# Performance work log

Hardware: AMD Instinct MI355X
Metric: run time of the kernel (lower is better)

Reference implementation:

```python
import jax, jax.numpy as jnp
import numpy as np

B, C_IN, T = 32, 192, 8192
H, N_PH, OUT = 192, 1024, 4
EPS = 1e-5


def setup_inputs() -> dict:
    key = jax.random.key(0)
    ks = jax.random.split(key, 12)
    s = 0.02
    return {
        "x": jax.random.normal(ks[0], (B, C_IN, T), jnp.float32),
        "x_mask": jnp.ones((B, 1, N_PH), jnp.float32),
        "w": jax.random.randint(ks[1], (B, 1, N_PH), 0, 8, jnp.int32),
        "pre_w": jax.random.normal(ks[2], (H, C_IN), jnp.float32) * s,
        "pre_b": jnp.zeros((H,), jnp.float32),
        "conv0_w": jax.random.normal(ks[3], (H, H, 3), jnp.float32) * s,
        "conv0_b": jnp.zeros((H,), jnp.float32),
        "ln0_g": jnp.ones((H,), jnp.float32),
        "ln0_b": jnp.zeros((H,), jnp.float32),
        "conv1_w": jax.random.normal(ks[4], (H, H, 3), jnp.float32) * s,
        "conv1_b": jnp.zeros((H,), jnp.float32),
        "ln1_g": jnp.ones((H,), jnp.float32),
        "ln1_b": jnp.zeros((H,), jnp.float32),
        "lin_w": jax.random.normal(ks[5], (OUT, H), jnp.float32) * s,
        "lin_b": jnp.zeros((OUT,), jnp.float32),
    }


def _segment_mean(x, w2):
    # x: [B, C, T] frames; w2: [B, n_ph] int durations.
    # Faithful to the torch double loop: phoneme j pools frames
    # [cumsum(w)[j-1] : cumsum(w)[j]); w==0 -> zeros.
    ends = jnp.cumsum(w2, axis=1)                      # [B, n_ph]
    t = jnp.arange(x.shape[2], dtype=ends.dtype)       # [T]
    ph_id = jax.vmap(lambda e: jnp.searchsorted(e, t, side="right"))(ends)  # [B, T]
    # segment sums over frames; extra segment n_ph catches out-of-range frames
    sums = jax.vmap(lambda xt, ids: jax.ops.segment_sum(xt, ids, num_segments=N_PH + 1))(
        x.transpose(0, 2, 1), ph_id
    )                                                  # [B, n_ph+1, C]
    sums = sums[:, :N_PH].transpose(0, 2, 1)           # [B, C, n_ph]
    denom = jnp.maximum(w2, 1).astype(x.dtype)[:, None, :]
    return jnp.where(w2[:, None, :] > 0, sums / denom, 0.0)


def _conv3(x, k, b):
    y = jax.lax.conv_general_dilated(x, k, (1,), [(1, 1)],
                                     dimension_numbers=("NCH", "OIH", "NCH"))
    return y + b[None, :, None]


def _ln(x, g, b):
    # channel-dim LayerNorm for [B, C, T] (VITS modules.LayerNorm)
    m = jnp.mean(x, axis=1, keepdims=True)
    v = jnp.mean(jnp.square(x - m), axis=1, keepdims=True)
    return (x - m) * jax.lax.rsqrt(v + EPS) * g[None, :, None] + b[None, :, None]


def reference(x, x_mask, w, pre_w, pre_b, conv0_w, conv0_b, ln0_g, ln0_b,
              conv1_w, conv1_b, ln1_g, ln1_b, lin_w, lin_b):
    w2 = w.reshape(w.shape[0], -1).astype(jnp.int32)
    spec = _segment_mean(x, w2)                                 # [B, C_in, n_ph]
    h = jnp.einsum("bct,hc->bht", spec, pre_w) + pre_b[None, :, None]
    # block 0: conv -> relu -> LN (dropout is identity at eval), mask before each layer
    h = _conv3(h * x_mask, conv0_w, conv0_b)
    h = jax.nn.relu(h * x_mask)
    h = _ln(h * x_mask, ln0_g, ln0_b)
    h = h * x_mask  # dropout(p=0.1) at eval = identity; mask still applied
    # block 1
    h = _conv3(h * x_mask, conv1_w, conv1_b)
    h = jax.nn.relu(h * x_mask)
    h = _ln(h * x_mask, ln1_g, ln1_b)
    h = h * x_mask
    p = jnp.einsum("bht,oh->bot", h, lin_w) + lin_b[None, :, None]
    return p * x_mask
```

## Files before the change

kernel.cpp:

```cpp
#include <hip/hip_runtime.h>
#include <hip/hip_bf16.h>

#define B 32
#define C_IN 192
#define T 8192
#define H 192
#define N_PH 1024
#define OUT 4
#define ROW_MAX 7168
#define PROWS (N_PH + 2)
#define ROWP (2 * H)

typedef __attribute__((ext_vector_type(8))) short short8;
typedef __attribute__((ext_vector_type(4))) float f32x4;
typedef unsigned short ushort_t;

__device__ inline ushort_t f2bf(float f) {
    unsigned u = __builtin_bit_cast(unsigned, f);
    unsigned r = u + 0x7fffu + ((u >> 16) & 1u);
    return (ushort_t)(r >> 16);
}
__device__ inline float bf2f(ushort_t h) {
    unsigned u = ((unsigned)h) << 16;
    return __builtin_bit_cast(float, u);
}
__device__ inline void split_bf(float x, ushort_t& hi, ushort_t& lo) {
    hi = f2bf(x);
    lo = f2bf(x - bf2f(hi));
}

__global__ __launch_bounds__(256) void segmean_kernel(const float* __restrict__ x,
                                                      const int* __restrict__ wdur,
                                                      float* __restrict__ spec) {
    int bc = blockIdx.x;
    int b = bc / C_IN;
    int c = bc % C_IN;
    __shared__ int e_s[N_PH];
    __shared__ int part[256];
    __shared__ float row[ROW_MAX];
    int tid = threadIdx.x;
    int4 w4 = ((const int4*)(wdur + b * N_PH))[tid];
    int c0 = w4.x, c1 = c0 + w4.y, c2 = c1 + w4.z, c3 = c2 + w4.w;
    part[tid] = c3;
    __syncthreads();
    for (int off = 1; off < 256; off <<= 1) {
        int v = (tid >= off) ? part[tid - off] : 0;
        __syncthreads();
        part[tid] += v;
        __syncthreads();
    }
    int pre = tid ? part[tid - 1] : 0;
    e_s[4 * tid + 0] = pre + c0;
    e_s[4 * tid + 1] = pre + c1;
    e_s[4 * tid + 2] = pre + c2;
    e_s[4 * tid + 3] = pre + c3;
    __syncthreads();
    int emax = e_s[N_PH - 1];
    const float4* xr4 = (const float4*)(x + ((size_t)b * C_IN + c) * T);
    float4* row4 = (float4*)row;
    int nv = (emax + 3) >> 2;
    for (int t = tid; t < nv; t += 256) row4[t] = xr4[t];
    __syncthreads();
    float* sp = spec + ((size_t)b * C_IN + c) * N_PH;
    for (int j = tid; j < N_PH; j += 256) {
        int s0 = j ? e_s[j - 1] : 0;
        int e0 = e_s[j];
        float sum = 0.f;
        for (int t = s0; t < e0; ++t) sum += row[t];
        sp[j] = (e0 > s0) ? sum / (float)(e0 - s0) : 0.f;
    }
}

__global__ __launch_bounds__(256) void transpose_spec_kernel(const float* __restrict__ spec,
                                                             ushort_t* __restrict__ specT) {
    int jt = blockIdx.x * 32;
    int ct = (blockIdx.y % (C_IN / 32)) * 32;
    int b  = blockIdx.y / (C_IN / 32);
    __shared__ float tile[32][33];
    int tx = threadIdx.x & 31;
    int ty = threadIdx.x >> 5;
    const float* sb = spec + ((size_t)b * C_IN + ct) * N_PH + jt;
    for (int r = ty; r < 32; r += 8) tile[r][tx] = sb[(size_t)r * N_PH + tx];
    __syncthreads();
    ushort_t* ob = specT + ((size_t)b * N_PH + jt) * ROWP + ct;
    for (int r = ty; r < 32; r += 8) {
        ushort_t hi, lo;
        split_bf(tile[tx][r], hi, lo);
        ob[(size_t)r * ROWP + tx] = hi;
        ob[(size_t)r * ROWP + H + tx] = lo;
    }
}

__device__ inline void wfrag_one(const float* __restrict__ w, ushort_t* __restrict__ wtf,
                                 int taps, int idx, int ntot) {
    int j  = idx & 7;
    int l  = (idx >> 3) & 63;
    int slot = idx >> 9;
    int nt = slot % 12;
    int ss = (slot / 12) % 6;
    int kt = slot / 72;
    int o  = nt * 16 + (l & 15);
    int i  = ss * 32 + ((l >> 4) << 3) + j;
    float v = (taps == 1) ? w[o * C_IN + i] : w[(o * H + i) * 3 + kt];
    ushort_t hi, lo;
    split_bf(v, hi, lo);
    wtf[idx] = hi;
    wtf[idx + ntot] = lo;
}
__global__ void wfrag_all_kernel(const float* __restrict__ pw, const float* __restrict__ w0,
                                 const float* __restrict__ w1,
                                 ushort_t* __restrict__ wpre, ushort_t* __restrict__ w0t,
                                 ushort_t* __restrict__ w1t) {
    int idx = blockIdx.x * 256 + threadIdx.x;
    const int n1 = 36864, n3 = 110592;
    if (idx < n1) { wfrag_one(pw, wpre, 1, idx, n1); return; }
    idx -= n1;
    if (idx < n3) { wfrag_one(w0, w0t, 3, idx, n3); return; }
    idx -= n3;
    if (idx < n3) wfrag_one(w1, w1t, 3, idx, n3);
}

#define LOADOPS(IT, AH0, AL0, AH1, AL1, BH, BL) do {                              \
    int kt_ = (IT) / 6, s_ = (IT) - kt_ * 6;                                      \
    const ushort_t* arow_ = inb + (long)(trow + kt_ - pad) * ROWP + s_ * 32 + kg; \
    AH0 = *(const short8*)(arow_);                                                \
    AL0 = *(const short8*)(arow_ + H);                                            \
    AH1 = *(const short8*)(arow_ + 16 * ROWP);                                    \
    AL1 = *(const short8*)(arow_ + 16 * ROWP + H);                                \
    const ushort_t* wb_ = wt + ((size_t)((kt_ * 6 + s_) * 12 + nhalf * 6) << 9)   \
                        + (lane << 3);                                            \
    _Pragma("unroll") for (int n_ = 0; n_ < 6; ++n_) {                            \
        BH[n_] = *(const short8*)(wb_ + (n_ << 9));                               \
        BL[n_] = *(const short8*)(wb_ + (n_ << 9) + ntotw); }                     \
} while (0)

#define DOMFMA(AH0, AL0, AH1, AL1, BH, BL) do {                                             \
    _Pragma("unroll") for (int n_ = 0; n_ < 6; ++n_) {                                      \
        acc[0][n_] = __builtin_amdgcn_mfma_f32_16x16x32_bf16(AH0, BH[n_], acc[0][n_], 0,0,0); \
        acc[0][n_] = __builtin_amdgcn_mfma_f32_16x16x32_bf16(AL0, BH[n_], acc[0][n_], 0,0,0); \
        acc[0][n_] = __builtin_amdgcn_mfma_f32_16x16x32_bf16(AH0, BL[n_], acc[0][n_], 0,0,0); \
        acc[1][n_] = __builtin_amdgcn_mfma_f32_16x16x32_bf16(AH1, BH[n_], acc[1][n_], 0,0,0); \
        acc[1][n_] = __builtin_amdgcn_mfma_f32_16x16x32_bf16(AL1, BH[n_], acc[1][n_], 0,0,0); \
        acc[1][n_] = __builtin_amdgcn_mfma_f32_16x16x32_bf16(AH1, BL[n_], acc[1][n_], 0,0,0); } \
} while (0)

__global__ __launch_bounds__(256) void gemm_fused_kernel(
    const ushort_t* __restrict__ in, int in_rows,
    const ushort_t* __restrict__ wt,
    const float* __restrict__ bias,
    const float* __restrict__ mask,
    const float* __restrict__ g, const float* __restrict__ beta,
    ushort_t* __restrict__ out,
    const float* __restrict__ lw, const float* __restrict__ lb,
    float* __restrict__ fout,
    int taps, int do_ln, int nmask, int fin)
{
    int b  = blockIdx.y;
    int t0 = blockIdx.x * 64;
    int tid = threadIdx.x;
    int lane = tid & 63;
    int wv = tid >> 6;
    int mhalf = wv & 1;
    int nhalf = wv >> 1;

    __shared__ float ep[64][193];
    __shared__ float g_s[H], b_s[H], m_s[64], mstat[64], rstat[64];
    if (tid < H) { g_s[tid] = do_ln ? g[tid] : 1.f; b_s[tid] = do_ln ? beta[tid] : 0.f; }
    if (tid < 64) m_s[tid] = mask[b * N_PH + t0 + tid];

    short8 z8 = {0, 0, 0, 0, 0, 0, 0, 0};
    if (!fin) {
        if (t0 == 0 && tid < ROWP / 8)
            *(short8*)(out + (size_t)b * PROWS * ROWP + tid * 8) = z8;
        if (t0 == N_PH - 64 && tid < ROWP / 8)
            *(short8*)(out + ((size_t)b * PROWS + N_PH + 1) * ROWP + tid * 8) = z8;
    }

    int m  = lane & 15;
    int kg = (lane >> 4) << 3;
    int ntotw = taps * 36864;
    int pad = taps >> 1;

    const ushort_t* inb = in + (size_t)b * in_rows * ROWP;
    int trow = t0 + mhalf * 32 + m;

    f32x4 acc[2][6];
#pragma unroll
    for (int ntl = 0; ntl < 6; ++ntl) {
        float bb = bias[(nhalf * 6 + ntl) * 16 + m];
        acc[0][ntl] = (f32x4){bb, bb, bb, bb};
        acc[1][ntl] = (f32x4){bb, bb, bb, bb};
    }

    short8 pah0, pal0, pah1, pal1, pbh[6], pbl[6];
    short8 qah0, qal0, qah1, qal1, qbh[6], qbl[6];
    int iters = taps * 6;
    LOADOPS(0, pah0, pal0, pah1, pal1, pbh, pbl);
#pragma unroll 1
    for (int it = 0; it < iters; it += 2) {
        LOADOPS(it + 1, qah0, qal0, qah1, qal1, qbh, qbl);
        DOMFMA(pah0, pal0, pah1, pal1, pbh, pbl);
        if (it + 2 < iters) LOADOPS(it + 2, pah0, pal0, pah1, pal1, pbh, pbl);
        DOMFMA(qah0, qal0, qah1, qal1, qbh, qbl);
    }

    __syncthreads();

    int rbase = (lane >> 4) << 2;
#pragma unroll
    for (int mh = 0; mh < 2; ++mh) {
#pragma unroll
        for (int ntl = 0; ntl < 6; ++ntl) {
            int o = (nhalf * 6 + ntl) * 16 + m;
#pragma unroll
            for (int r = 0; r < 4; ++r) {
                int t_loc = mhalf * 32 + mh * 16 + rbase + r;
                float mm = m_s[t_loc];
                float v = acc[mh][ntl][r];
                if (do_ln) {
                    v = fmaxf(v * mm, 0.f) * mm;
                } else {
                    for (int q = 0; q < nmask; ++q) v *= mm;
                }
                ep[t_loc][o] = v;
            }
        }
    }
    __syncthreads();

    if (do_ln && tid < 64) {
        float s = 0.f, ss = 0.f;
        for (int c = 0; c < H; ++c) {
            float v = ep[tid][c];
            s += v;
            ss += v * v;
        }
        float mean = s * (1.f / (float)H);
        mstat[tid] = mean;
        rstat[tid] = rsqrtf(ss * (1.f / (float)H) - mean * mean + 1e-5f);
    }
    __syncthreads();

    int row = tid >> 2;
    int q = tid & 3;
    if (fin) {
        float mean = mstat[row], rstd = rstat[row], mk = m_s[row];
        float a0 = 0.f, a1 = 0.f, a2 = 0.f, a3 = 0.f;
#pragma unroll 1
        for (int c = q * 48; c < q * 48 + 48; ++c) {
            float y = ((ep[row][c] - mean) * rstd * g_s[c] + b_s[c]) * mk;
            a0 += lw[0 * H + c] * y;
            a1 += lw[1 * H + c] * y;
            a2 += lw[2 * H + c] * y;
            a3 += lw[3 * H + c] * y;
        }
        a0 += __shfl_xor(a0, 1); a0 += __shfl_xor(a0, 2);
        a1 += __shfl_xor(a1, 1); a1 += __shfl_xor(a1, 2);
        a2 += __shfl_xor(a2, 1); a2 += __shfl_xor(a2, 2);
        a3 += __shfl_xor(a3, 1); a3 += __shfl_xor(a3, 2);
        if (q == 0) {
            int t = t0 + row;
            float* ob = fout + (size_t)b * OUT * N_PH + t;
            ob[0 * N_PH] = (a0 + lb[0]) * mk;
            ob[1 * N_PH] = (a1 + lb[1]) * mk;
            ob[2 * N_PH] = (a2 + lb[2]) * mk;
            ob[3 * N_PH] = (a3 + lb[3]) * mk;
        }
        return;
    }

    float mean = 0.f, rstd = 1.f, mfac = 1.f;
    if (do_ln) {
        mean = mstat[row];
        rstd = rstat[row];
        float mk = m_s[row];
        mfac = (nmask == 2) ? mk * mk : mk;
    }
    ushort_t* orow = out + ((size_t)b * PROWS + t0 + row + 1) * ROWP + q * 48;
#pragma unroll
    for (int i0 = 0; i0 < 48; i0 += 8) {
        ushort_t th[8], tl[8];
#pragma unroll
        for (int k2 = 0; k2 < 8; ++k2) {
            int c = q * 48 + i0 + k2;
            float v = ep[row][c];
            float y = do_ln ? ((v - mean) * rstd * g_s[c] + b_s[c]) * mfac : v;
            split_bf(y, th[k2], tl[k2]);
        }
        *(short8*)(orow + i0) = *(short8*)th;
        *(short8*)(orow + H + i0) = *(short8*)tl;
    }
}

extern "C" void kernel_launch(void* const* d_in, const int* in_sizes, int n_in,
                              void* d_out, int out_size, void* d_ws, size_t ws_size,
                              hipStream_t stream) {
    const float* x      = (const float*)d_in[0];
    const float* x_mask = (const float*)d_in[1];
    const int*   w      = (const int*)d_in[2];
    const float* pre_w  = (const float*)d_in[3];
    const float* pre_b  = (const float*)d_in[4];
    const float* conv0_w = (const float*)d_in[5];
    const float* conv0_b = (const float*)d_in[6];
    const float* ln0_g   = (const float*)d_in[7];
    const float* ln0_b   = (const float*)d_in[8];
    const float* conv1_w = (const float*)d_in[9];
    const float* conv1_b = (const float*)d_in[10];
    const float* ln1_g   = (const float*)d_in[11];
    const float* ln1_b   = (const float*)d_in[12];
    const float* lin_w   = (const float*)d_in[13];
    const float* lin_b   = (const float*)d_in[14];
    float* out = (float*)d_out;

    char* ws = (char*)d_ws;
    size_t off = 0;
    float* spec = (float*)(ws + off);       off += (size_t)B * C_IN * N_PH * sizeof(float);
    ushort_t* bufA = (ushort_t*)(ws + off); off += (size_t)B * PROWS * ROWP * sizeof(ushort_t);
    ushort_t* bufB = (ushort_t*)(ws + off); off += (size_t)B * PROWS * ROWP * sizeof(ushort_t);
    ushort_t* wpre = (ushort_t*)(ws + off); off += (size_t)2 * 36864 * sizeof(ushort_t);
    ushort_t* w0t  = (ushort_t*)(ws + off); off += (size_t)2 * 110592 * sizeof(ushort_t);
    ushort_t* w1t  = (ushort_t*)(ws + off); off += (size_t)2 * 110592 * sizeof(ushort_t);
    ushort_t* specT = bufB;

    wfrag_all_kernel<<<(36864 + 2 * 110592 + 255) / 256, 256, 0, stream>>>(
        pre_w, conv0_w, conv1_w, wpre, w0t, w1t);

    segmean_kernel<<<B * C_IN, 256, 0, stream>>>(x, w, spec);
    dim3 gt(N_PH / 32, (C_IN / 32) * B);
    transpose_spec_kernel<<<gt, 256, 0, stream>>>(spec, specT);

    dim3 gg(N_PH / 64, B);
    gemm_fused_kernel<<<gg, 256, 0, stream>>>(specT, N_PH, wpre, pre_b, x_mask,
                                              ln0_g, ln0_b, bufA,
                                              nullptr, nullptr, nullptr, 1, 0, 1, 0);
    gemm_fused_kernel<<<gg, 256, 0, stream>>>(bufA + ROWP, PROWS, w0t, conv0_b, x_mask,
                                              ln0_g, ln0_b, bufB,
                                              nullptr, nullptr, nullptr, 3, 1, 2, 0);
    gemm_fused_kernel<<<gg, 256, 0, stream>>>(bufB + ROWP, PROWS, w1t, conv1_b, x_mask,
                                              ln1_g, ln1_b, bufA,
                                              lin_w, lin_b, out, 3, 1, 1, 1);
}
```

Before: 397.6 us.

## Fuse segment-mean with transpose and halve GEMM row tile to 32

```diff
diff --git a/kernel.cpp b/kernel.cpp
--- a/kernel.cpp
+++ b/kernel.cpp
@@ -29,19 +29,19 @@
     lo = f2bf(x - bf2f(hi));
 }
 
-__global__ __launch_bounds__(256) void segmean_kernel(const float* __restrict__ x,
-                                                      const int* __restrict__ wdur,
-                                                      float* __restrict__ spec) {
-    int bc = blockIdx.x;
-    int b = bc / C_IN;
-    int c = bc % C_IN;
+__global__ __launch_bounds__(256) void segmeanT_kernel(const float* __restrict__ x,
+                                                       const int* __restrict__ wdur,
+                                                       ushort_t* __restrict__ specT) {
+    int b   = blockIdx.y;
+    int jt0 = blockIdx.x * 32;
     __shared__ int e_s[N_PH];
     __shared__ int part[256];
-    __shared__ float row[ROW_MAX];
+    __shared__ __align__(16) float tile[32][225];
+    __shared__ __align__(16) ushort_t resh[32][32], resl[32][32];
     int tid = threadIdx.x;
     int4 w4 = ((const int4*)(wdur + b * N_PH))[tid];
-    int c0 = w4.x, c1 = c0 + w4.y, c2 = c1 + w4.z, c3 = c2 + w4.w;
-    part[tid] = c3;
+    int c0s = w4.x, c1s = c0s + w4.y, c2s = c1s + w4.z, c3s = c2s + w4.w;
+    part[tid] = c3s;
     __syncthreads();
     for (int off = 1; off < 256; off <<= 1) {
         int v = (tid >= off) ? part[tid - off] : 0;
@@ -50,44 +50,47 @@
         __syncthreads();
     }
     int pre = tid ? part[tid - 1] : 0;
-    e_s[4 * tid + 0] = pre + c0;
-    e_s[4 * tid + 1] = pre + c1;
-    e_s[4 * tid + 2] = pre + c2;
-    e_s[4 * tid + 3] = pre + c3;
-    __syncthreads();
-    int emax = e_s[N_PH - 1];
-    const float4* xr4 = (const float4*)(x + ((size_t)b * C_IN + c) * T);
-    float4* row4 = (float4*)row;
-    int nv = (emax + 3) >> 2;
-    for (int t = tid; t < nv; t += 256) row4[t] = xr4[t];
-    __syncthreads();
-    float* sp = spec + ((size_t)b * C_IN + c) * N_PH;
-    for (int j = tid; j < N_PH; j += 256) {
-        int s0 = j ? e_s[j - 1] : 0;
-        int e0 = e_s[j];
-        float sum = 0.f;
-        for (int t = s0; t < e0; ++t) sum += row[t];
-        sp[j] = (e0 > s0) ? sum / (float)(e0 - s0) : 0.f;
-    }
-}
-
-__global__ __launch_bounds__(256) void transpose_spec_kernel(const float* __restrict__ spec,
-                                                             ushort_t* __restrict__ specT) {
-    int jt = blockIdx.x * 32;
-    int ct = (blockIdx.y % (C_IN / 32)) * 32;
-    int b  = blockIdx.y / (C_IN / 32);
-    __shared__ float tile[32][33];
-    int tx = threadIdx.x & 31;
-    int ty = threadIdx.x >> 5;
-    const float* sb = spec + ((size_t)b * C_IN + ct) * N_PH + jt;
-    for (int r = ty; r < 32; r += 8) tile[r][tx] = sb[(size_t)r * N_PH + tx];
-    __syncthreads();
-    ushort_t* ob = specT + ((size_t)b * N_PH + jt) * ROWP + ct;
-    for (int r = ty; r < 32; r += 8) {
-        ushort_t hi, lo;
-        split_bf(tile[tx][r], hi, lo);
-        ob[(size_t)r * ROWP + tx] = hi;
-        ob[(size_t)r * ROWP + H + tx] = lo;
+    e_s[4 * tid + 0] = pre + c0s;
+    e_s[4 * tid + 1] = pre + c1s;
+    e_s[4 * tid + 2] = pre + c2s;
+    e_s[4 * tid + 3] = pre + c3s;
+    __syncthreads();
+    int s_base = jt0 ? e_s[jt0 - 1] : 0;
+    int nf = e_s[jt0 + 31] - s_base;
+    int wv = tid >> 6, lane = tid & 63;
+    int j_loc = tid & 31;
+    int j = jt0 + j_loc;
+    int s0 = j ? e_s[j - 1] : 0;
+    int e0 = e_s[j];
+    int fs = s0 - s_base, fe = e0 - s_base;
+    float inv = (e0 > s0) ? 1.f / (float)(e0 - s0) : 0.f;
+    int cb = (tid >> 5) * 4;
+    for (int hh = 0; hh < 6; ++hh) {
+        int c0 = hh * 32;
+        for (int cl = wv; cl < 32; cl += 4) {
+            const float* xr = x + ((size_t)b * C_IN + c0 + cl) * T + s_base;
+            for (int f = lane; f < nf; f += 64) tile[cl][f] = xr[f];
+        }
+        __syncthreads();
+        for (int cc = 0; cc < 4; ++cc) {
+            int cl = cb + cc;
+            float sum = 0.f;
+            for (int f = fs; f < fe; ++f) sum += tile[cl][f];
+            ushort_t hi, lo;
+            split_bf(sum * inv, hi, lo);
+            resh[j_loc][cl] = hi;
+            resl[j_loc][cl] = lo;
+        }
+        __syncthreads();
+        {
+            int row = tid >> 3, k = tid & 7;
+            int plane = k >> 2, ch = (k & 3) * 8;
+            ushort_t* dst = specT + ((size_t)b * N_PH + jt0 + row) * ROWP
+                          + plane * H + c0 + ch;
+            const ushort_t* src = plane ? &resl[row][ch] : &resh[row][ch];
+            *(short8*)dst = *(short8*)src;
+        }
+        __syncthreads();
     }
 }
 
@@ -120,30 +123,6 @@
     if (idx < n3) wfrag_one(w1, w1t, 3, idx, n3);
 }
 
-#define LOADOPS(IT, AH0, AL0, AH1, AL1, BH, BL) do {                              \
-    int kt_ = (IT) / 6, s_ = (IT) - kt_ * 6;                                      \
-    const ushort_t* arow_ = inb + (long)(trow + kt_ - pad) * ROWP + s_ * 32 + kg; \
-    AH0 = *(const short8*)(arow_);                                                \
-    AL0 = *(const short8*)(arow_ + H);                                            \
-    AH1 = *(const short8*)(arow_ + 16 * ROWP);                                    \
-    AL1 = *(const short8*)(arow_ + 16 * ROWP + H);                                \
-    const ushort_t* wb_ = wt + ((size_t)((kt_ * 6 + s_) * 12 + nhalf * 6) << 9)   \
-                        + (lane << 3);                                            \
-    _Pragma("unroll") for (int n_ = 0; n_ < 6; ++n_) {                            \
-        BH[n_] = *(const short8*)(wb_ + (n_ << 9));                               \
-        BL[n_] = *(const short8*)(wb_ + (n_ << 9) + ntotw); }                     \
-} while (0)
-
-#define DOMFMA(AH0, AL0, AH1, AL1, BH, BL) do {                                             \
-    _Pragma("unroll") for (int n_ = 0; n_ < 6; ++n_) {                                      \
-        acc[0][n_] = __builtin_amdgcn_mfma_f32_16x16x32_bf16(AH0, BH[n_], acc[0][n_], 0,0,0); \
-        acc[0][n_] = __builtin_amdgcn_mfma_f32_16x16x32_bf16(AL0, BH[n_], acc[0][n_], 0,0,0); \
-        acc[0][n_] = __builtin_amdgcn_mfma_f32_16x16x32_bf16(AH0, BL[n_], acc[0][n_], 0,0,0); \
-        acc[1][n_] = __builtin_amdgcn_mfma_f32_16x16x32_bf16(AH1, BH[n_], acc[1][n_], 0,0,0); \
-        acc[1][n_] = __builtin_amdgcn_mfma_f32_16x16x32_bf16(AL1, BH[n_], acc[1][n_], 0,0,0); \
-        acc[1][n_] = __builtin_amdgcn_mfma_f32_16x16x32_bf16(AH1, BL[n_], acc[1][n_], 0,0,0); } \
-} while (0)
-
 __global__ __launch_bounds__(256) void gemm_fused_kernel(
     const ushort_t* __restrict__ in, int in_rows,
     const ushort_t* __restrict__ wt,
@@ -156,23 +135,23 @@
     int taps, int do_ln, int nmask, int fin)
 {
     int b  = blockIdx.y;
-    int t0 = blockIdx.x * 64;
+    int t0 = blockIdx.x * 32;
     int tid = threadIdx.x;
     int lane = tid & 63;
     int wv = tid >> 6;
     int mhalf = wv & 1;
     int nhalf = wv >> 1;
 
-    __shared__ float ep[64][193];
-    __shared__ float g_s[H], b_s[H], m_s[64], mstat[64], rstat[64];
+    __shared__ float ep[32][193];
+    __shared__ float g_s[H], b_s[H], m_s[32], mstat[32], rstat[32];
     if (tid < H) { g_s[tid] = do_ln ? g[tid] : 1.f; b_s[tid] = do_ln ? beta[tid] : 0.f; }
-    if (tid < 64) m_s[tid] = mask[b * N_PH + t0 + tid];
+    if (tid < 32) m_s[tid] = mask[b * N_PH + t0 + tid];
 
     short8 z8 = {0, 0, 0, 0, 0, 0, 0, 0};
     if (!fin) {
         if (t0 == 0 && tid < ROWP / 8)
             *(short8*)(out + (size_t)b * PROWS * ROWP + tid * 8) = z8;
-        if (t0 == N_PH - 64 && tid < ROWP / 8)
+        if (t0 == N_PH - 32 && tid < ROWP / 8)
             *(short8*)(out + ((size_t)b * PROWS + N_PH + 1) * ROWP + tid * 8) = z8;
     }
 
@@ -182,53 +161,82 @@
     int pad = taps >> 1;
 
     const ushort_t* inb = in + (size_t)b * in_rows * ROWP;
-    int trow = t0 + mhalf * 32 + m;
-
-    f32x4 acc[2][6];
+    int trow = t0 + mhalf * 16 + m;
+
+    f32x4 acc[6];
 #pragma unroll
     for (int ntl = 0; ntl < 6; ++ntl) {
         float bb = bias[(nhalf * 6 + ntl) * 16 + m];
-        acc[0][ntl] = (f32x4){bb, bb, bb, bb};
-        acc[1][ntl] = (f32x4){bb, bb, bb, bb};
-    }
-
-    short8 pah0, pal0, pah1, pal1, pbh[6], pbl[6];
-    short8 qah0, qal0, qah1, qal1, qbh[6], qbl[6];
+        acc[ntl] = (f32x4){bb, bb, bb, bb};
+    }
+
     int iters = taps * 6;
-    LOADOPS(0, pah0, pal0, pah1, pal1, pbh, pbl);
+    short8 pah, pal, qah, qal;
+    {
+        const ushort_t* ar = inb + (long)(trow - pad) * ROWP + kg;
+        pah = *(const short8*)(ar);
+        pal = *(const short8*)(ar + H);
+    }
 #pragma unroll 1
     for (int it = 0; it < iters; it += 2) {
-        LOADOPS(it + 1, qah0, qal0, qah1, qal1, qbh, qbl);
-        DOMFMA(pah0, pal0, pah1, pal1, pbh, pbl);
-        if (it + 2 < iters) LOADOPS(it + 2, pah0, pal0, pah1, pal1, pbh, pbl);
-        DOMFMA(qah0, qal0, qah1, qal1, qbh, qbl);
+        {
+            int i1 = it + 1, kt = i1 / 6, s = i1 - kt * 6;
+            const ushort_t* ar = inb + (long)(trow + kt - pad) * ROWP + s * 32 + kg;
+            qah = *(const short8*)(ar);
+            qal = *(const short8*)(ar + H);
+        }
+        {
+            const ushort_t* wb = wt + ((size_t)(it * 12 + nhalf * 6) << 9) + (lane << 3);
+#pragma unroll
+            for (int n = 0; n < 6; ++n) {
+                short8 bh = *(const short8*)(wb + (n << 9));
+                short8 bl = *(const short8*)(wb + (n << 9) + ntotw);
+                acc[n] = __builtin_amdgcn_mfma_f32_16x16x32_bf16(pah, bh, acc[n], 0, 0, 0);
+                acc[n] = __builtin_amdgcn_mfma_f32_16x16x32_bf16(pal, bh, acc[n], 0, 0, 0);
+                acc[n] = __builtin_amdgcn_mfma_f32_16x16x32_bf16(pah, bl, acc[n], 0, 0, 0);
+            }
+        }
+        if (it + 2 < iters) {
+            int i2 = it + 2, kt = i2 / 6, s = i2 - kt * 6;
+            const ushort_t* ar = inb + (long)(trow + kt - pad) * ROWP + s * 32 + kg;
+            pah = *(const short8*)(ar);
+            pal = *(const short8*)(ar + H);
+        }
+        {
+            const ushort_t* wb = wt + ((size_t)((it + 1) * 12 + nhalf * 6) << 9) + (lane << 3);
+#pragma unroll
+            for (int n = 0; n < 6; ++n) {
+                short8 bh = *(const short8*)(wb + (n << 9));
+                short8 bl = *(const short8*)(wb + (n << 9) + ntotw);
+                acc[n] = __builtin_amdgcn_mfma_f32_16x16x32_bf16(qah, bh, acc[n], 0, 0, 0);
+                acc[n] = __builtin_amdgcn_mfma_f32_16x16x32_bf16(qal, bh, acc[n], 0, 0, 0);
+                acc[n] = __builtin_amdgcn_mfma_f32_16x16x32_bf16(qah, bl, acc[n], 0, 0, 0);
+            }
+        }
     }
 
     __syncthreads();
 
     int rbase = (lane >> 4) << 2;
 #pragma unroll
-    for (int mh = 0; mh < 2; ++mh) {
-#pragma unroll
-        for (int ntl = 0; ntl < 6; ++ntl) {
-            int o = (nhalf * 6 + ntl) * 16 + m;
-#pragma unroll
-            for (int r = 0; r < 4; ++r) {
-                int t_loc = mhalf * 32 + mh * 16 + rbase + r;
-                float mm = m_s[t_loc];
-                float v = acc[mh][ntl][r];
-                if (do_ln) {
-                    v = fmaxf(v * mm, 0.f) * mm;
-                } else {
-                    for (int q = 0; q < nmask; ++q) v *= mm;
-                }
-                ep[t_loc][o] = v;
+    for (int ntl = 0; ntl < 6; ++ntl) {
+        int o = (nhalf * 6 + ntl) * 16 + m;
+#pragma unroll
+        for (int r = 0; r < 4; ++r) {
+            int t_loc = mhalf * 16 + rbase + r;
+            float mm = m_s[t_loc];
+            float v = acc[ntl][r];
+            if (do_ln) {
+                v = fmaxf(v * mm, 0.f) * mm;
+            } else {
+                for (int q = 0; q < nmask; ++q) v *= mm;
             }
-        }
-    }
-    __syncthreads();
-
-    if (do_ln && tid < 64) {
+            ep[t_loc][o] = v;
+        }
+    }
+    __syncthreads();
+
+    if (do_ln && tid < 32) {
         float s = 0.f, ss = 0.f;
         for (int c = 0; c < H; ++c) {
             float v = ep[tid][c];
@@ -241,23 +249,23 @@
     }
     __syncthreads();
 
-    int row = tid >> 2;
-    int q = tid & 3;
+    int row = tid >> 3;
+    int q = tid & 7;
     if (fin) {
         float mean = mstat[row], rstd = rstat[row], mk = m_s[row];
         float a0 = 0.f, a1 = 0.f, a2 = 0.f, a3 = 0.f;
 #pragma unroll 1
-        for (int c = q * 48; c < q * 48 + 48; ++c) {
+        for (int c = q * 24; c < q * 24 + 24; ++c) {
             float y = ((ep[row][c] - mean) * rstd * g_s[c] + b_s[c]) * mk;
             a0 += lw[0 * H + c] * y;
             a1 += lw[1 * H + c] * y;
             a2 += lw[2 * H + c] * y;
             a3 += lw[3 * H + c] * y;
         }
-        a0 += __shfl_xor(a0, 1); a0 += __shfl_xor(a0, 2);
-        a1 += __shfl_xor(a1, 1); a1 += __shfl_xor(a1, 2);
-        a2 += __shfl_xor(a2, 1); a2 += __shfl_xor(a2, 2);
-        a3 += __shfl_xor(a3, 1); a3 += __shfl_xor(a3, 2);
+        a0 += __shfl_xor(a0, 1); a0 += __shfl_xor(a0, 2); a0 += __shfl_xor(a0, 4);
+        a1 += __shfl_xor(a1, 1); a1 += __shfl_xor(a1, 2); a1 += __shfl_xor(a1, 4);
+        a2 += __shfl_xor(a2, 1); a2 += __shfl_xor(a2, 2); a2 += __shfl_xor(a2, 4);
+        a3 += __shfl_xor(a3, 1); a3 += __shfl_xor(a3, 2); a3 += __shfl_xor(a3, 4);
         if (q == 0) {
             int t = t0 + row;
             float* ob = fout + (size_t)b * OUT * N_PH + t;
@@ -276,13 +284,13 @@
         float mk = m_s[row];
         mfac = (nmask == 2) ? mk * mk : mk;
     }
-    ushort_t* orow = out + ((size_t)b * PROWS + t0 + row + 1) * ROWP + q * 48;
-#pragma unroll
-    for (int i0 = 0; i0 < 48; i0 += 8) {
+    ushort_t* orow = out + ((size_t)b * PROWS + t0 + row + 1) * ROWP + q * 24;
+#pragma unroll
+    for (int i0 = 0; i0 < 24; i0 += 8) {
         ushort_t th[8], tl[8];
 #pragma unroll
         for (int k2 = 0; k2 < 8; ++k2) {
-            int c = q * 48 + i0 + k2;
+            int c = q * 24 + i0 + k2;
             float v = ep[row][c];
             float y = do_ln ? ((v - mean) * rstd * g_s[c] + b_s[c]) * mfac : v;
             split_bf(y, th[k2], tl[k2]);
@@ -314,7 +322,6 @@
 
     char* ws = (char*)d_ws;
     size_t off = 0;
-    float* spec = (float*)(ws + off);       off += (size_t)B * C_IN * N_PH * sizeof(float);
     ushort_t* bufA = (ushort_t*)(ws + off); off += (size_t)B * PROWS * ROWP * sizeof(ushort_t);
     ushort_t* bufB = (ushort_t*)(ws + off); off += (size_t)B * PROWS * ROWP * sizeof(ushort_t);
     ushort_t* wpre = (ushort_t*)(ws + off); off += (size_t)2 * 36864 * sizeof(ushort_t);
@@ -325,11 +332,10 @@
     wfrag_all_kernel<<<(36864 + 2 * 110592 + 255) / 256, 256, 0, stream>>>(
         pre_w, conv0_w, conv1_w, wpre, w0t, w1t);
 
-    segmean_kernel<<<B * C_IN, 256, 0, stream>>>(x, w, spec);
-    dim3 gt(N_PH / 32, (C_IN / 32) * B);
-    transpose_spec_kernel<<<gt, 256, 0, stream>>>(spec, specT);
-
-    dim3 gg(N_PH / 64, B);
+    dim3 gs(N_PH / 32, B);
+    segmeanT_kernel<<<gs, 256, 0, stream>>>(x, w, specT);
+
+    dim3 gg(N_PH / 32, B);
     gemm_fused_kernel<<<gg, 256, 0, stream>>>(specT, N_PH, wpre, pre_b, x_mask,
                                               ln0_g, ln0_b, bufA,
                                               nullptr, nullptr, nullptr, 1, 0, 1, 0);
```

After: 476.8 us. +19.9%, slower.
